# Optimization experiments

Measured on AMD Instinct MI355X. Metric: run time of the kernel, lower is better.

The kernel has to match this reference:

```python
import jax, jax.numpy as jnp
import numpy as np

N = 100000      # nodes
E = 1600000     # edges (avg degree 16)
DIN = 3         # input_dim (xyz coords)
DOUT = 64       # output_dim
EPS = 1e-5      # LayerNorm eps


def setup_inputs() -> dict:
    key = jax.random.key(0)
    ks = jax.random.split(key, 6)
    x = jax.random.normal(ks[0], (N, DIN), jnp.float32)
    edge_index = jax.random.randint(ks[1], (2, E), 0, N, dtype=jnp.int64)
    # li1: Linear(DIN, DOUT)
    W1 = jax.random.normal(ks[2], (DIN, DOUT), jnp.float32) / np.sqrt(DIN)
    b1 = jnp.zeros((DOUT,), jnp.float32)
    # gcn1: GCNConv(DOUT, DOUT) -> weight + bias
    Wg = jax.random.normal(ks[3], (DOUT, DOUT), jnp.float32) / np.sqrt(DOUT)
    bg = jnp.zeros((DOUT,), jnp.float32)
    # norm1d: LayerNorm(2*DOUT)
    gamma = jnp.ones((2 * DOUT,), jnp.float32)
    beta = jnp.zeros((2 * DOUT,), jnp.float32)
    return {"x": x, "edge_index": edge_index, "W1": W1, "b1": b1,
            "Wg": Wg, "bg": bg, "gamma": gamma, "beta": beta}


def reference(x, edge_index, W1, b1, Wg, bg, gamma, beta):
    n = x.shape[0]
    # li1 + act
    h = jax.nn.relu(x @ W1 + b1)                       # [N, DOUT]
    # GCNConv: add self loops, symmetric normalization D^-1/2 (A+I) D^-1/2
    loops = jnp.arange(n, dtype=edge_index.dtype)
    src = jnp.concatenate([edge_index[0], loops])      # [E+N]
    dst = jnp.concatenate([edge_index[1], loops])      # [E+N]
    deg = jax.ops.segment_sum(jnp.ones_like(dst, h.dtype), dst, num_segments=n)
    dinv = jnp.where(deg > 0, jax.lax.rsqrt(jnp.maximum(deg, 1.0)), 0.0)
    norm = dinv[src] * dinv[dst]                       # [E+N]
    hg = h @ Wg                                        # [N, DOUT]
    agg = jax.ops.segment_sum(hg[src] * norm[:, None], dst, num_segments=n)
    h2 = jax.nn.relu(agg + bg)                         # [N, DOUT]
    # concat + LayerNorm(2*DOUT)
    cat = jnp.concatenate([h, h2], axis=1)             # [N, 2*DOUT]
    mu = jnp.mean(cat, axis=-1, keepdims=True)
    var = jnp.mean(jnp.square(cat - mu), axis=-1, keepdims=True)
    return (cat - mu) * jax.lax.rsqrt(var + EPS) * gamma + beta
```

## Files before the change

kernel.cpp:

```cpp
#include <hip/hip_runtime.h>
#include <math.h>

#define N_NODES 100000
#define N_EDGES 1600000
#define EPS_    1e-5f
#define PAD     64
#define SCOL    48


#define NCHUNK_E 782
#define EPB_E    2048
#define NB_EDGE  (NCHUNK_E * 8)
#define PART_SZ  12500

#define LIN_WAVES 1563
#define NB_LIN    391

typedef float v16f __attribute__((ext_vector_type(16)));

__device__ __forceinline__ float bf2f(unsigned short u) {
    union { unsigned int i; float f; } v; v.i = (unsigned int)u << 16; return v.f;
}
__device__ __forceinline__ unsigned short f2bf(float f) {
    union { float f; unsigned int i; } v; v.f = f;
    unsigned int b = v.i + 0x7FFFu + ((v.i >> 16) & 1u);
    return (unsigned short)(b >> 16);
}
__device__ __forceinline__ unsigned int pk2(float lo, float hi) {
    return (unsigned int)f2bf(lo) | ((unsigned int)f2bf(hi) << 16);
}

__global__ void edge_kernel(const int* __restrict__ src,
                            const int* __restrict__ dst,
                            int* __restrict__ cnt,
                            int* __restrict__ ell)
{
    const int part  = blockIdx.x & 7;
    const int chunk = blockIdx.x >> 3;
    const int lo    = part * PART_SZ;
    const int hi    = lo + PART_SZ;

    const int ebase = chunk * EPB_E + threadIdx.x * 8;
    int dv[8], sv[8];
    if (ebase + 8 <= N_EDGES) {
        const int4 d0 = *(const int4*)(dst + ebase);
        const int4 d1 = *(const int4*)(dst + ebase + 4);
        const int4 s0 = *(const int4*)(src + ebase);
        const int4 s1 = *(const int4*)(src + ebase + 4);
        dv[0] = d0.x; dv[1] = d0.y; dv[2] = d0.z; dv[3] = d0.w;
        dv[4] = d1.x; dv[5] = d1.y; dv[6] = d1.z; dv[7] = d1.w;
        sv[0] = s0.x; sv[1] = s0.y; sv[2] = s0.z; sv[3] = s0.w;
        sv[4] = s1.x; sv[5] = s1.y; sv[6] = s1.z; sv[7] = s1.w;
    } else {
#pragma unroll
        for (int j = 0; j < 8; ++j) {
            const int e = ebase + j;
            if (e < N_EDGES) { dv[j] = dst[e]; sv[j] = src[e]; }
            else             { dv[j] = -1;     sv[j] = 0;      }
        }
    }

#pragma unroll
    for (int j = 0; j < 8; ++j) {
        if (dv[j] >= lo && dv[j] < hi) {
            const int pos = atomicAdd(&cnt[dv[j]], 1);
            if (pos < PAD) ell[dv[j] * PAD + pos] = sv[j];
        }
    }
}

#define FMA16(A, wv0, wv1, wv2, wv3)                                          \
    do {                                                                      \
        A[0]  = fmaf(hk, wv0.x, A[0]);  A[1]  = fmaf(hk, wv0.y, A[1]);        \
        A[2]  = fmaf(hk, wv0.z, A[2]);  A[3]  = fmaf(hk, wv0.w, A[3]);        \
        A[4]  = fmaf(hk, wv1.x, A[4]);  A[5]  = fmaf(hk, wv1.y, A[5]);        \
        A[6]  = fmaf(hk, wv1.z, A[6]);  A[7]  = fmaf(hk, wv1.w, A[7]);        \
        A[8]  = fmaf(hk, wv2.x, A[8]);  A[9]  = fmaf(hk, wv2.y, A[9]);        \
        A[10] = fmaf(hk, wv2.z, A[10]); A[11] = fmaf(hk, wv2.w, A[11]);       \
        A[12] = fmaf(hk, wv3.x, A[12]); A[13] = fmaf(hk, wv3.y, A[13]);       \
        A[14] = fmaf(hk, wv3.z, A[14]); A[15] = fmaf(hk, wv3.w, A[15]);       \
    } while (0)

__global__ void lin_kernel(const float* __restrict__ x,
                           const float* __restrict__ W1,
                           const float* __restrict__ b1,
                           const float* __restrict__ Wg,
                           unsigned short* __restrict__ hb_g)
{
    const int tl   = threadIdx.x;
    const int wave = blockIdx.x * 4 + (tl >> 6);
    if (wave >= LIN_WAVES) return;

    const int lane = tl & 63;
    const int n    = wave * 64 + lane;
    const bool act = (n < N_NODES);
    float x0 = 0.f, x1 = 0.f, x2 = 0.f;
    if (act) { x0 = x[n * 3]; x1 = x[n * 3 + 1]; x2 = x[n * 3 + 2]; }

    v16f a0, a1, a2, a3;
#pragma unroll
    for (int i = 0; i < 16; ++i) { a0[i] = 0.f; a1[i] = 0.f; a2[i] = 0.f; a3[i] = 0.f; }

    for (int k = 0; k < 64; ++k) {
        const float w0 = W1[k];
        const float w1 = W1[64 + k];
        const float w2 = W1[128 + k];
        const float bb = b1[k];
        const float hk = fmaxf(fmaf(x0, w0, fmaf(x1, w1, fmaf(x2, w2, bb))), 0.f);

        const float4* __restrict__ r4 = (const float4*)(Wg + (size_t)k * 64);
        const float4 p0 = r4[0],  p1 = r4[1],  p2 = r4[2],  p3 = r4[3];
        const float4 p4 = r4[4],  p5 = r4[5],  p6 = r4[6],  p7 = r4[7];
        const float4 p8 = r4[8],  p9 = r4[9],  pa = r4[10], pb = r4[11];
        const float4 pc = r4[12], pd = r4[13], pe = r4[14], pf = r4[15];

        FMA16(a0, p0, p1, p2, p3);
        FMA16(a1, p4, p5, p6, p7);
        FMA16(a2, p8, p9, pa, pb);
        FMA16(a3, pc, pd, pe, pf);
    }

    if (act) {
        uint4* __restrict__ dp = (uint4*)(hb_g + (size_t)n * 64);
        dp[0] = make_uint4(pk2(a0[0],  a0[1]),  pk2(a0[2],  a0[3]),
                           pk2(a0[4],  a0[5]),  pk2(a0[6],  a0[7]));
        dp[1] = make_uint4(pk2(a0[8],  a0[9]),  pk2(a0[10], a0[11]),
                           pk2(a0[12], a0[13]), pk2(a0[14], a0[15]));
        dp[2] = make_uint4(pk2(a1[0],  a1[1]),  pk2(a1[2],  a1[3]),
                           pk2(a1[4],  a1[5]),  pk2(a1[6],  a1[7]));
        dp[3] = make_uint4(pk2(a1[8],  a1[9]),  pk2(a1[10], a1[11]),
                           pk2(a1[12], a1[13]), pk2(a1[14], a1[15]));
        dp[4] = make_uint4(pk2(a2[0],  a2[1]),  pk2(a2[2],  a2[3]),
                           pk2(a2[4],  a2[5]),  pk2(a2[6],  a2[7]));
        dp[5] = make_uint4(pk2(a2[8],  a2[9]),  pk2(a2[10], a2[11]),
                           pk2(a2[12], a2[13]), pk2(a2[14], a2[15]));
        dp[6] = make_uint4(pk2(a3[0],  a3[1]),  pk2(a3[2],  a3[3]),
                           pk2(a3[4],  a3[5]),  pk2(a3[6],  a3[7]));
        dp[7] = make_uint4(pk2(a3[8],  a3[9]),  pk2(a3[10], a3[11]),
                           pk2(a3[12], a3[13]), pk2(a3[14], a3[15]));
    }
}

__global__ void scale_kernel(const int* __restrict__ cnt,
                             unsigned int* __restrict__ g2)
{
    const int t = blockIdx.x * blockDim.x + threadIdx.x;
    if (t >= N_NODES * 32) return;
    const int node = t >> 5;
    const float di = rsqrtf((float)(cnt[node] + 1));
    const unsigned int v = g2[t];
    const float lo = bf2f((unsigned short)(v & 0xFFFFu)) * di;
    const float hi = bf2f((unsigned short)(v >> 16)) * di;
    g2[t] = (unsigned int)f2bf(lo) | ((unsigned int)f2bf(hi) << 16);
}

__global__ void gather_final_kernel(const unsigned short* __restrict__ hb_g,
                                    const int* __restrict__ cnt,
                                    const int* __restrict__ ell,
                                    const float* __restrict__ x,
                                    const float* __restrict__ W1,
                                    const float* __restrict__ b1,
                                    const float* __restrict__ bg,
                                    const float* __restrict__ gamma,
                                    const float* __restrict__ beta,
                                    float* __restrict__ out)
{
    __shared__ int sell[64 * SCOL];
    __shared__ int lcnt[64];
    const int tl = threadIdx.x;
    const int b  = blockIdx.x;
    const int nb = b * 64;

    if (tl < 64) {
        const int n = nb + tl;
        lcnt[tl] = (n < N_NODES) ? cnt[n] : 0;
    }
    {
        const int r = tl >> 2;
        const int q = tl & 3;
        const int nr = nb + r;
        if (nr < N_NODES) {
            const int4* __restrict__ grow = (const int4*)(ell + (size_t)nr * PAD);
            int4* __restrict__ srow = (int4*)(sell + r * SCOL);
            srow[q]     = grow[q];
            srow[q + 4] = grow[q + 4];
            srow[q + 8] = grow[q + 8];
        }
    }
    __syncthreads();

    const int lane = tl & 63;
    const int w    = tl >> 6;
    const float w0 = W1[lane], w1 = W1[64 + lane], w2 = W1[128 + lane];
    const float bb1 = b1[lane];
    const float bgl = bg[lane];
    const float g0 = gamma[lane], g1 = gamma[64 + lane];
    const float be0 = beta[lane], be1 = beta[64 + lane];

    for (int nl = w; nl < 64; nl += 4) {
        const int n = nb + nl;
        if (n >= N_NODES) break;

        const int c    = lcnt[nl];
        const float di = rsqrtf((float)(c + 1));
        const int deg  = (c < PAD) ? c : PAD;
        const int dstg = (deg < SCOL) ? deg : SCOL;
        const int* row = sell + nl * SCOL;

        const float xx0 = x[n * 3], xx1 = x[n * 3 + 1], xx2 = x[n * 3 + 2];
        float acc = bf2f(hb_g[(size_t)n * 64 + lane]);

        int j = 0;
        for (; j + 8 <= dstg; j += 8) {
            const int s0 = row[j + 0], s1 = row[j + 1], s2 = row[j + 2], s3 = row[j + 3];
            const int s4 = row[j + 4], s5 = row[j + 5], s6 = row[j + 6], s7 = row[j + 7];
            const float a0 = bf2f(hb_g[(size_t)s0 * 64 + lane]);
            const float a1 = bf2f(hb_g[(size_t)s1 * 64 + lane]);
            const float a2 = bf2f(hb_g[(size_t)s2 * 64 + lane]);
            const float a3 = bf2f(hb_g[(size_t)s3 * 64 + lane]);
            const float a4 = bf2f(hb_g[(size_t)s4 * 64 + lane]);
            const float a5 = bf2f(hb_g[(size_t)s5 * 64 + lane]);
            const float a6 = bf2f(hb_g[(size_t)s6 * 64 + lane]);
            const float a7 = bf2f(hb_g[(size_t)s7 * 64 + lane]);
            acc += ((a0 + a1) + (a2 + a3)) + ((a4 + a5) + (a6 + a7));
        }
        if (j + 4 <= dstg) {
            const int s0 = row[j + 0], s1 = row[j + 1], s2 = row[j + 2], s3 = row[j + 3];
            acc += (bf2f(hb_g[(size_t)s0 * 64 + lane]) + bf2f(hb_g[(size_t)s1 * 64 + lane]))
                 + (bf2f(hb_g[(size_t)s2 * 64 + lane]) + bf2f(hb_g[(size_t)s3 * 64 + lane]));
            j += 4;
        }
        for (; j < dstg; ++j) acc += bf2f(hb_g[(size_t)row[j] * 64 + lane]);
        for (; j < deg; ++j)
            acc += bf2f(hb_g[(size_t)ell[(size_t)n * PAD + j] * 64 + lane]);

        float h  = fmaxf(fmaf(xx0, w0, fmaf(xx1, w1, fmaf(xx2, w2, bb1))), 0.f);
        float h2 = fmaxf(fmaf(di, acc, bgl), 0.f);

        float sum = h + h2;
#pragma unroll
        for (int o = 32; o > 0; o >>= 1) sum += __shfl_xor(sum, o, 64);
        const float mu = sum * (1.0f / 128.0f);

        const float dA = h  - mu;
        const float dB = h2 - mu;
        float vs = dA * dA + dB * dB;
#pragma unroll
        for (int o = 32; o > 0; o >>= 1) vs += __shfl_xor(vs, o, 64);
        const float rr = rsqrtf(vs * (1.0f / 128.0f) + EPS_);

        out[(size_t)n * 128 + lane]      = dA * rr * g0 + be0;
        out[(size_t)n * 128 + 64 + lane] = dB * rr * g1 + be1;
    }
}

extern "C" void kernel_launch(void* const* d_in, const int* in_sizes, int n_in,
                              void* d_out, int out_size, void* d_ws, size_t ws_size,
                              hipStream_t stream)
{
    const float* x     = (const float*)d_in[0];
    const int*   edge  = (const int*)  d_in[1];
    const float* W1    = (const float*)d_in[2];
    const float* b1    = (const float*)d_in[3];
    const float* Wg    = (const float*)d_in[4];
    const float* bg    = (const float*)d_in[5];
    const float* gamma = (const float*)d_in[6];
    const float* beta  = (const float*)d_in[7];
    float*       out   = (float*)d_out;

    char*  ws  = (char*)d_ws;
    size_t p   = 0;
    unsigned short* hb_g = (unsigned short*)(ws + p); p += (size_t)N_NODES * 64 * sizeof(unsigned short);
    int*            ell  = (int*)           (ws + p); p += (size_t)N_NODES * PAD * sizeof(int);
    int*            cnt  = (int*)           (ws + p);

    const int* src = edge;
    const int* dst = edge + N_EDGES;

    hipMemsetAsync(cnt, 0, (size_t)N_NODES * sizeof(int), stream);

    edge_kernel<<<NB_EDGE, 256, 0, stream>>>(src, dst, cnt, ell);
    lin_kernel <<<NB_LIN,  256, 0, stream>>>(x, W1, b1, Wg, hb_g);
    scale_kernel<<<(N_NODES * 32 + 255) / 256, 256, 0, stream>>>(cnt, (unsigned int*)hb_g);
    gather_final_kernel<<<(N_NODES + 63) / 64, 256, 0, stream>>>(hb_g, cnt, ell,
                                                                 x, W1, b1,
                                                                 bg, gamma, beta, out);
}
```

Baseline: 249.0 us.

## Fuse edge bucketing with linear transform and apply source normalization during gather

Merges the edge-bucketing kernel and the node linear/GCN-weight kernel into one launch: blocks first issue their degree atomics, then the first waves compute the bf16 hidden features, then write the ELL entries. This lets the atomic latency overlap the matmul work. The separate scale kernel is dropped, and the gather now multiplies each neighbour's feature by rsqrt of that neighbour's degree, read per edge from the count array. That removes a full read-modify-write pass over the feature buffer, but adds a random count load and an rsqrt per edge in the gather. It also skips a second bf16 rounding of the scaled features.

```diff
diff --git a/kernel.cpp b/kernel.cpp
--- a/kernel.cpp
+++ b/kernel.cpp
@@ -14,7 +14,6 @@
 #define PART_SZ  12500
 
 #define LIN_WAVES 1563
-#define NB_LIN    391
 
 typedef float v16f __attribute__((ext_vector_type(16)));
 
@@ -28,45 +27,6 @@
 }
 __device__ __forceinline__ unsigned int pk2(float lo, float hi) {
     return (unsigned int)f2bf(lo) | ((unsigned int)f2bf(hi) << 16);
-}
-
-__global__ void edge_kernel(const int* __restrict__ src,
-                            const int* __restrict__ dst,
-                            int* __restrict__ cnt,
-                            int* __restrict__ ell)
-{
-    const int part  = blockIdx.x & 7;
-    const int chunk = blockIdx.x >> 3;
-    const int lo    = part * PART_SZ;
-    const int hi    = lo + PART_SZ;
-
-    const int ebase = chunk * EPB_E + threadIdx.x * 8;
-    int dv[8], sv[8];
-    if (ebase + 8 <= N_EDGES) {
-        const int4 d0 = *(const int4*)(dst + ebase);
-        const int4 d1 = *(const int4*)(dst + ebase + 4);
-        const int4 s0 = *(const int4*)(src + ebase);
-        const int4 s1 = *(const int4*)(src + ebase + 4);
-        dv[0] = d0.x; dv[1] = d0.y; dv[2] = d0.z; dv[3] = d0.w;
-        dv[4] = d1.x; dv[5] = d1.y; dv[6] = d1.z; dv[7] = d1.w;
-        sv[0] = s0.x; sv[1] = s0.y; sv[2] = s0.z; sv[3] = s0.w;
-        sv[4] = s1.x; sv[5] = s1.y; sv[6] = s1.z; sv[7] = s1.w;
-    } else {
-#pragma unroll
-        for (int j = 0; j < 8; ++j) {
-            const int e = ebase + j;
-            if (e < N_EDGES) { dv[j] = dst[e]; sv[j] = src[e]; }
-            else             { dv[j] = -1;     sv[j] = 0;      }
-        }
-    }
-
-#pragma unroll
-    for (int j = 0; j < 8; ++j) {
-        if (dv[j] >= lo && dv[j] < hi) {
-            const int pos = atomicAdd(&cnt[dv[j]], 1);
-            if (pos < PAD) ell[dv[j] * PAD + pos] = sv[j];
-        }
-    }
 }
 
 #define FMA16(A, wv0, wv1, wv2, wv3)                                          \
@@ -81,77 +41,109 @@
         A[14] = fmaf(hk, wv3.z, A[14]); A[15] = fmaf(hk, wv3.w, A[15]);       \
     } while (0)
 
-__global__ void lin_kernel(const float* __restrict__ x,
-                           const float* __restrict__ W1,
-                           const float* __restrict__ b1,
-                           const float* __restrict__ Wg,
-                           unsigned short* __restrict__ hb_g)
+__global__ void fused_edge_lin_kernel(const int* __restrict__ src,
+                                      const int* __restrict__ dst,
+                                      const float* __restrict__ x,
+                                      const float* __restrict__ W1,
+                                      const float* __restrict__ b1,
+                                      const float* __restrict__ Wg,
+                                      int* __restrict__ cnt,
+                                      int* __restrict__ ell,
+                                      unsigned short* __restrict__ hb_g)
 {
-    const int tl   = threadIdx.x;
+    const int tl    = threadIdx.x;
+    const int part  = blockIdx.x & 7;
+    const int chunk = blockIdx.x >> 3;
+    const int lo    = part * PART_SZ;
+    const int hi    = lo + PART_SZ;
+
+    const int ebase = chunk * EPB_E + tl * 8;
+    int dv[8], sv[8], pos[8];
+    if (ebase + 8 <= N_EDGES) {
+        const int4 d0 = *(const int4*)(dst + ebase);
+        const int4 d1 = *(const int4*)(dst + ebase + 4);
+        const int4 s0 = *(const int4*)(src + ebase);
+        const int4 s1 = *(const int4*)(src + ebase + 4);
+        dv[0] = d0.x; dv[1] = d0.y; dv[2] = d0.z; dv[3] = d0.w;
+        dv[4] = d1.x; dv[5] = d1.y; dv[6] = d1.z; dv[7] = d1.w;
+        sv[0] = s0.x; sv[1] = s0.y; sv[2] = s0.z; sv[3] = s0.w;
+        sv[4] = s1.x; sv[5] = s1.y; sv[6] = s1.z; sv[7] = s1.w;
+    } else {
+#pragma unroll
+        for (int j = 0; j < 8; ++j) {
+            const int e = ebase + j;
+            if (e < N_EDGES) { dv[j] = dst[e]; sv[j] = src[e]; }
+            else             { dv[j] = -1;     sv[j] = 0;      }
+        }
+    }
+#pragma unroll
+    for (int j = 0; j < 8; ++j) {
+        pos[j] = -1;
+        if (dv[j] >= lo && dv[j] < hi) pos[j] = atomicAdd(&cnt[dv[j]], 1);
+    }
+
     const int wave = blockIdx.x * 4 + (tl >> 6);
-    if (wave >= LIN_WAVES) return;
-
-    const int lane = tl & 63;
-    const int n    = wave * 64 + lane;
-    const bool act = (n < N_NODES);
-    float x0 = 0.f, x1 = 0.f, x2 = 0.f;
-    if (act) { x0 = x[n * 3]; x1 = x[n * 3 + 1]; x2 = x[n * 3 + 2]; }
-
-    v16f a0, a1, a2, a3;
-#pragma unroll
-    for (int i = 0; i < 16; ++i) { a0[i] = 0.f; a1[i] = 0.f; a2[i] = 0.f; a3[i] = 0.f; }
-
-    for (int k = 0; k < 64; ++k) {
-        const float w0 = W1[k];
-        const float w1 = W1[64 + k];
-        const float w2 = W1[128 + k];
-        const float bb = b1[k];
-        const float hk = fmaxf(fmaf(x0, w0, fmaf(x1, w1, fmaf(x2, w2, bb))), 0.f);
-
-        const float4* __restrict__ r4 = (const float4*)(Wg + (size_t)k * 64);
-        const float4 p0 = r4[0],  p1 = r4[1],  p2 = r4[2],  p3 = r4[3];
-        const float4 p4 = r4[4],  p5 = r4[5],  p6 = r4[6],  p7 = r4[7];
-        const float4 p8 = r4[8],  p9 = r4[9],  pa = r4[10], pb = r4[11];
-        const float4 pc = r4[12], pd = r4[13], pe = r4[14], pf = r4[15];
-
-        FMA16(a0, p0, p1, p2, p3);
-        FMA16(a1, p4, p5, p6, p7);
-        FMA16(a2, p8, p9, pa, pb);
-        FMA16(a3, pc, pd, pe, pf);
-    }
-
-    if (act) {
-        uint4* __restrict__ dp = (uint4*)(hb_g + (size_t)n * 64);
-        dp[0] = make_uint4(pk2(a0[0],  a0[1]),  pk2(a0[2],  a0[3]),
-                           pk2(a0[4],  a0[5]),  pk2(a0[6],  a0[7]));
-        dp[1] = make_uint4(pk2(a0[8],  a0[9]),  pk2(a0[10], a0[11]),
-                           pk2(a0[12], a0[13]), pk2(a0[14], a0[15]));
-        dp[2] = make_uint4(pk2(a1[0],  a1[1]),  pk2(a1[2],  a1[3]),
-                           pk2(a1[4],  a1[5]),  pk2(a1[6],  a1[7]));
-        dp[3] = make_uint4(pk2(a1[8],  a1[9]),  pk2(a1[10], a1[11]),
-                           pk2(a1[12], a1[13]), pk2(a1[14], a1[15]));
-        dp[4] = make_uint4(pk2(a2[0],  a2[1]),  pk2(a2[2],  a2[3]),
-                           pk2(a2[4],  a2[5]),  pk2(a2[6],  a2[7]));
-        dp[5] = make_uint4(pk2(a2[8],  a2[9]),  pk2(a2[10], a2[11]),
-                           pk2(a2[12], a2[13]), pk2(a2[14], a2[15]));
-        dp[6] = make_uint4(pk2(a3[0],  a3[1]),  pk2(a3[2],  a3[3]),
-                           pk2(a3[4],  a3[5]),  pk2(a3[6],  a3[7]));
-        dp[7] = make_uint4(pk2(a3[8],  a3[9]),  pk2(a3[10], a3[11]),
-                           pk2(a3[12], a3[13]), pk2(a3[14], a3[15]));
-    }
-}
-
-__global__ void scale_kernel(const int* __restrict__ cnt,
-                             unsigned int* __restrict__ g2)
-{
-    const int t = blockIdx.x * blockDim.x + threadIdx.x;
-    if (t >= N_NODES * 32) return;
-    const int node = t >> 5;
-    const float di = rsqrtf((float)(cnt[node] + 1));
-    const unsigned int v = g2[t];
-    const float lo = bf2f((unsigned short)(v & 0xFFFFu)) * di;
-    const float hi = bf2f((unsigned short)(v >> 16)) * di;
-    g2[t] = (unsigned int)f2bf(lo) | ((unsigned int)f2bf(hi) << 16);
+    if (wave < LIN_WAVES) {
+        const int lane = tl & 63;
+        const int n    = wave * 64 + lane;
+        const bool act = (n < N_NODES);
+        float x0 = 0.f, x1 = 0.f, x2 = 0.f;
+        if (act) { x0 = x[n * 3]; x1 = x[n * 3 + 1]; x2 = x[n * 3 + 2]; }
+
+        v16f a0, a1, a2, a3;
+#pragma unroll
+        for (int i = 0; i < 16; ++i) { a0[i] = 0.f; a1[i] = 0.f; a2[i] = 0.f; a3[i] = 0.f; }
+
+        for (int k = 0; k < 64; ++k) {
+            const float w0 = W1[k];
+            const float w1 = W1[64 + k];
+            const float w2 = W1[128 + k];
+            const float bb = b1[k];
+            const float hk = fmaxf(fmaf(x0, w0, fmaf(x1, w1, fmaf(x2, w2, bb))), 0.f);
+
+            const float4* __restrict__ r4 = (const float4*)(Wg + (size_t)k * 64);
+            {
+                const float4 p0 = r4[0], p1 = r4[1], p2 = r4[2], p3 = r4[3];
+                FMA16(a0, p0, p1, p2, p3);
+            }
+            {
+                const float4 p0 = r4[4], p1 = r4[5], p2 = r4[6], p3 = r4[7];
+                FMA16(a1, p0, p1, p2, p3);
+            }
+            {
+                const float4 p0 = r4[8], p1 = r4[9], p2 = r4[10], p3 = r4[11];
+                FMA16(a2, p0, p1, p2, p3);
+            }
+            {
+                const float4 p0 = r4[12], p1 = r4[13], p2 = r4[14], p3 = r4[15];
+                FMA16(a3, p0, p1, p2, p3);
+            }
+        }
+
+        if (act) {
+            uint4* __restrict__ dp = (uint4*)(hb_g + (size_t)n * 64);
+            dp[0] = make_uint4(pk2(a0[0],  a0[1]),  pk2(a0[2],  a0[3]),
+                               pk2(a0[4],  a0[5]),  pk2(a0[6],  a0[7]));
+            dp[1] = make_uint4(pk2(a0[8],  a0[9]),  pk2(a0[10], a0[11]),
+                               pk2(a0[12], a0[13]), pk2(a0[14], a0[15]));
+            dp[2] = make_uint4(pk2(a1[0],  a1[1]),  pk2(a1[2],  a1[3]),
+                               pk2(a1[4],  a1[5]),  pk2(a1[6],  a1[7]));
+            dp[3] = make_uint4(pk2(a1[8],  a1[9]),  pk2(a1[10], a1[11]),
+                               pk2(a1[12], a1[13]), pk2(a1[14], a1[15]));
+            dp[4] = make_uint4(pk2(a2[0],  a2[1]),  pk2(a2[2],  a2[3]),
+                               pk2(a2[4],  a2[5]),  pk2(a2[6],  a2[7]));
+            dp[5] = make_uint4(pk2(a2[8],  a2[9]),  pk2(a2[10], a2[11]),
+                               pk2(a2[12], a2[13]), pk2(a2[14], a2[15]));
+            dp[6] = make_uint4(pk2(a3[0],  a3[1]),  pk2(a3[2],  a3[3]),
+                               pk2(a3[4],  a3[5]),  pk2(a3[6],  a3[7]));
+            dp[7] = make_uint4(pk2(a3[8],  a3[9]),  pk2(a3[10], a3[11]),
+                               pk2(a3[12], a3[13]), pk2(a3[14], a3[15]));
+        }
+    }
+
+#pragma unroll
+    for (int j = 0; j < 8; ++j)
+        if (pos[j] >= 0 && pos[j] < PAD) ell[dv[j] * PAD + pos[j]] = sv[j];
 }
 
 __global__ void gather_final_kernel(const unsigned short* __restrict__ hb_g,
@@ -208,7 +200,7 @@
         const int* row = sell + nl * SCOL;
 
         const float xx0 = x[n * 3], xx1 = x[n * 3 + 1], xx2 = x[n * 3 + 2];
-        float acc = bf2f(hb_g[(size_t)n * 64 + lane]);
+        float acc = di * bf2f(hb_g[(size_t)n * 64 + lane]);
 
         int j = 0;
         for (; j + 8 <= dstg; j += 8) {
@@ -222,17 +214,29 @@
             const float a5 = bf2f(hb_g[(size_t)s5 * 64 + lane]);
             const float a6 = bf2f(hb_g[(size_t)s6 * 64 + lane]);
             const float a7 = bf2f(hb_g[(size_t)s7 * 64 + lane]);
-            acc += ((a0 + a1) + (a2 + a3)) + ((a4 + a5) + (a6 + a7));
-        }
-        if (j + 4 <= dstg) {
-            const int s0 = row[j + 0], s1 = row[j + 1], s2 = row[j + 2], s3 = row[j + 3];
-            acc += (bf2f(hb_g[(size_t)s0 * 64 + lane]) + bf2f(hb_g[(size_t)s1 * 64 + lane]))
-                 + (bf2f(hb_g[(size_t)s2 * 64 + lane]) + bf2f(hb_g[(size_t)s3 * 64 + lane]));
-            j += 4;
-        }
-        for (; j < dstg; ++j) acc += bf2f(hb_g[(size_t)row[j] * 64 + lane]);
-        for (; j < deg; ++j)
-            acc += bf2f(hb_g[(size_t)ell[(size_t)n * PAD + j] * 64 + lane]);
+            const float v0 = rsqrtf((float)(cnt[s0] + 1));
+            const float v1 = rsqrtf((float)(cnt[s1] + 1));
+            const float v2 = rsqrtf((float)(cnt[s2] + 1));
+            const float v3 = rsqrtf((float)(cnt[s3] + 1));
+            const float v4 = rsqrtf((float)(cnt[s4] + 1));
+            const float v5 = rsqrtf((float)(cnt[s5] + 1));
+            const float v6 = rsqrtf((float)(cnt[s6] + 1));
+            const float v7 = rsqrtf((float)(cnt[s7] + 1));
+            acc = fmaf(v0, a0, acc); acc = fmaf(v1, a1, acc);
+            acc = fmaf(v2, a2, acc); acc = fmaf(v3, a3, acc);
+            acc = fmaf(v4, a4, acc); acc = fmaf(v5, a5, acc);
+            acc = fmaf(v6, a6, acc); acc = fmaf(v7, a7, acc);
+        }
+        for (; j < dstg; ++j) {
+            const int s = row[j];
+            acc = fmaf(rsqrtf((float)(cnt[s] + 1)),
+                       bf2f(hb_g[(size_t)s * 64 + lane]), acc);
+        }
+        for (; j < deg; ++j) {
+            const int s = ell[(size_t)n * PAD + j];
+            acc = fmaf(rsqrtf((float)(cnt[s] + 1)),
+                       bf2f(hb_g[(size_t)s * 64 + lane]), acc);
+        }
 
         float h  = fmaxf(fmaf(xx0, w0, fmaf(xx1, w1, fmaf(xx2, w2, bb1))), 0.f);
         float h2 = fmaxf(fmaf(di, acc, bgl), 0.f);
@@ -279,9 +283,8 @@
 
     hipMemsetAsync(cnt, 0, (size_t)N_NODES * sizeof(int), stream);
 
-    edge_kernel<<<NB_EDGE, 256, 0, stream>>>(src, dst, cnt, ell);
-    lin_kernel <<<NB_LIN,  256, 0, stream>>>(x, W1, b1, Wg, hb_g);
-    scale_kernel<<<(N_NODES * 32 + 255) / 256, 256, 0, stream>>>(cnt, (unsigned int*)hb_g);
+    fused_edge_lin_kernel<<<NB_EDGE, 256, 0, stream>>>(src, dst, x, W1, b1, Wg,
+                                                       cnt, ell, hb_g);
     gather_final_kernel<<<(N_NODES + 63) / 64, 256, 0, stream>>>(hb_g, cnt, ell,
                                                                  x, W1, b1,
                                                                  bg, gamma, beta, out);
```

Result: faster. 239.1 us (-4.0%).
